# Performance work log

Measured on AMD Instinct MI355X. Metric: run time of the kernel, lower is better.

The kernel has to match this reference:

```python
import jax, jax.numpy as jnp
import numpy as np

N_NODES = 50000
N_EDGES = 800000
IN_DIM = 128
OUT_DIM = 64
LEAKY_SLOPE = 0.01  # torch F.leaky_relu default


def setup_inputs() -> dict:
    key = jax.random.key(0)
    k1, k2, k3, k4, k5 = jax.random.split(key, 5)
    features = jax.random.normal(k1, (N_NODES, IN_DIM), dtype=jnp.float32)
    src = jax.random.randint(k2, (N_EDGES,), 0, N_NODES, dtype=jnp.int32)
    dst = jax.random.randint(k3, (N_EDGES,), 0, N_NODES, dtype=jnp.int32)
    # fc: Linear(in_dim, out_dim, bias=False) -> stored as [in_dim, out_dim]
    W_fc = jax.random.normal(k4, (IN_DIM, OUT_DIM), dtype=jnp.float32) * (1.0 / np.sqrt(IN_DIM))
    # attn_fc: Linear(2*out_dim, 1, bias=False) -> stored as flat [2*out_dim]
    a_vec = jax.random.normal(k5, (2 * OUT_DIM,), dtype=jnp.float32) * (1.0 / np.sqrt(2 * OUT_DIM))
    return {"features": features, "src": src, "dst": dst, "W_fc": W_fc, "a_vec": a_vec}


def reference(features, src, dst, W_fc, a_vec):
    n = features.shape[0]
    d = W_fc.shape[1]
    # node projection: z = fc(features)
    z = features @ W_fc                                   # [N, d]
    # attn score: a^T [z_src || z_dst] = (z @ a_src)[src] + (z @ a_dst)[dst]
    az_src = z @ a_vec[:d]                                # [N]
    az_dst = z @ a_vec[d:]                                # [N]
    e = jax.nn.leaky_relu(az_src[src] + az_dst[dst], negative_slope=LEAKY_SLOPE)  # [E]
    # segment softmax over edges grouped by destination node
    e_max = jax.ops.segment_max(e, dst, num_segments=n)   # [N] (-inf for isolated nodes)
    e_exp = jnp.exp(e - e_max[dst])                       # [E]
    e_sum = jax.ops.segment_sum(e_exp, dst, num_segments=n)  # [N]
    alpha = e_exp / e_sum[dst]                            # [E]
    # weighted scatter-sum of source features to destination nodes
    h = jax.ops.segment_sum(alpha[:, None] * z[src], dst, num_segments=n)  # [N, d]
    return h
```

## Files before the change

kernel.cpp:

```cpp
#include <hip/hip_runtime.h>
#include <hip/hip_bf16.h>
#include <math.h>

#define N_NODES 50000
#define N_EDGES 800000
#define IN_DIM  128
#define OUT_DIM 64
#define LEAKY   0.01f

#define PROJ_ROWS 64
#define PROJ_NB   ((N_NODES + PROJ_ROWS - 1) / PROJ_ROWS)

#define SCAN_B   1024
#define SCAN_NB  ((N_NODES + SCAN_B - 1) / SCAN_B)

__global__ __launch_bounds__(256) void proj_kernel(
        const float* __restrict__ feat, const float* __restrict__ W,
        const float* __restrict__ a,
        __hip_bfloat16* __restrict__ zb,
        float* __restrict__ az_src, float* __restrict__ az_dst) {
    __shared__ float fs[PROJ_ROWS * IN_DIM];
    int tid  = threadIdx.x;
    int row0 = blockIdx.x * PROJ_ROWS;
    int nrows = N_NODES - row0; if (nrows > PROJ_ROWS) nrows = PROJ_ROWS;

    const float4* gsrc = (const float4*)(feat + (size_t)row0 * IN_DIM);
    if (nrows == PROJ_ROWS) {
#pragma unroll
        for (int i = 0; i < 8; ++i) {
            int idx = tid + i * 256;
            ((float4*)fs)[idx] = gsrc[idx];
        }
    } else {
        int lim = nrows * (IN_DIM / 4);
#pragma unroll
        for (int i = 0; i < 8; ++i) {
            int idx = tid + i * 256;
            if (idx < lim) ((float4*)fs)[idx] = gsrc[idx];
        }
    }
    __syncthreads();

    int lane  = tid & 63;
    int rbase = (tid >> 6) * 16;

    float acc[16];
#pragma unroll
    for (int r = 0; r < 16; ++r) acc[r] = 0.f;

    for (int kk = 0; kk < IN_DIM / 4; ++kk) {
        float w0 = W[(kk * 4 + 0) * OUT_DIM + lane];
        float w1 = W[(kk * 4 + 1) * OUT_DIM + lane];
        float w2 = W[(kk * 4 + 2) * OUT_DIM + lane];
        float w3 = W[(kk * 4 + 3) * OUT_DIM + lane];
#pragma unroll
        for (int r = 0; r < 16; ++r) {
            float4 f = *(const float4*)&fs[(rbase + r) * IN_DIM + kk * 4];
            acc[r] = fmaf(f.x, w0, acc[r]);
            acc[r] = fmaf(f.y, w1, acc[r]);
            acc[r] = fmaf(f.z, w2, acc[r]);
            acc[r] = fmaf(f.w, w3, acc[r]);
        }
    }

    float a1 = a[lane], a2 = a[OUT_DIM + lane];
#pragma unroll
    for (int r = 0; r < 16; ++r) {
        int row = row0 + rbase + r;
        if (row < N_NODES) {
            zb[(size_t)row * OUT_DIM + lane] = __float2bfloat16(acc[r]);
            float s1 = acc[r] * a1;
            float s2 = acc[r] * a2;
#pragma unroll
            for (int off = 32; off > 0; off >>= 1) {
                s1 += __shfl_xor(s1, off, 64);
                s2 += __shfl_xor(s2, off, 64);
            }
            if (lane == r) { az_src[row] = s1; az_dst[row] = s2; }
        }
    }
}

__global__ __launch_bounds__(256) void hist_kernel(
        const int* __restrict__ dst, int* __restrict__ counts,
        int* __restrict__ rank) {
    int i = blockIdx.x * 256 + threadIdx.x;
    if (i < N_EDGES) rank[i] = atomicAdd(&counts[dst[i]], 1);
}

__global__ __launch_bounds__(SCAN_B) void scan1_kernel(
        const int* __restrict__ counts, int* __restrict__ offsets,
        int* __restrict__ blocksums) {
    __shared__ int s[SCAN_B];
    int i = blockIdx.x * SCAN_B + threadIdx.x;
    int v = (i < N_NODES) ? counts[i] : 0;
    s[threadIdx.x] = v;
    __syncthreads();
    for (int off = 1; off < SCAN_B; off <<= 1) {
        int t = (threadIdx.x >= off) ? s[threadIdx.x - off] : 0;
        __syncthreads();
        s[threadIdx.x] += t;
        __syncthreads();
    }
    if (i < N_NODES) offsets[i] = s[threadIdx.x] - v;
    if (threadIdx.x == SCAN_B - 1) blocksums[blockIdx.x] = s[SCAN_B - 1];
}

__global__ __launch_bounds__(SCAN_B) void scan3_kernel(
        int* __restrict__ offsets, const int* __restrict__ blocksums) {
    __shared__ int bs[64];
    if (threadIdx.x < 64) {
        int lane = threadIdx.x;
        int v = (lane < SCAN_NB) ? blocksums[lane] : 0;
        int inc = v;
#pragma unroll
        for (int off = 1; off < 64; off <<= 1) {
            int t = __shfl_up(inc, off, 64);
            if (lane >= off) inc += t;
        }
        bs[lane] = inc - v;
    }
    __syncthreads();
    int i = blockIdx.x * SCAN_B + threadIdx.x;
    if (i < N_NODES) offsets[i] += bs[blockIdx.x];
    if (i == 0) offsets[N_NODES] = N_EDGES;
}

__global__ __launch_bounds__(256) void build_csr_kernel(
        const int* __restrict__ src, const int* __restrict__ dst,
        const int* __restrict__ rank, const int* __restrict__ offsets,
        int* __restrict__ src_sorted) {
    int i = blockIdx.x * 256 + threadIdx.x;
    if (i >= N_EDGES) return;
    int t = dst[i];
    int pos = offsets[t] + rank[i];
    src_sorted[pos] = src[i];
}

__global__ __launch_bounds__(256) void node_fused_kernel(
        const int* __restrict__ offsets, const int* __restrict__ src_sorted,
        const float* __restrict__ az_src, const float* __restrict__ az_dst,
        const __hip_bfloat16* __restrict__ zb, float* __restrict__ h) {
    int lane = threadIdx.x & 63;
    int w    = threadIdx.x >> 6;
    int t    = blockIdx.x * 4 + w;
    if (t >= N_NODES) return;
    int beg = offsets[t];
    int end = offsets[t + 1];
    float az_d = az_dst[t];

    float acc0 = 0.f, acc1 = 0.f, acc2 = 0.f, acc3 = 0.f;
    float ss0 = 0.f, ss1 = 0.f, ss2 = 0.f, ss3 = 0.f;
    int i = beg;
    for (; i + 4 <= end; i += 4) {
        int s0 = src_sorted[i];
        int s1 = src_sorted[i + 1];
        int s2 = src_sorted[i + 2];
        int s3 = src_sorted[i + 3];
        float v0 = az_src[s0] + az_d;
        float v1 = az_src[s1] + az_d;
        float v2 = az_src[s2] + az_d;
        float v3 = az_src[s3] + az_d;
        v0 = v0 > 0.f ? v0 : LEAKY * v0;
        v1 = v1 > 0.f ? v1 : LEAKY * v1;
        v2 = v2 > 0.f ? v2 : LEAKY * v2;
        v3 = v3 > 0.f ? v3 : LEAKY * v3;
        float x0 = __expf(v0), x1 = __expf(v1);
        float x2 = __expf(v2), x3 = __expf(v3);
        ss0 += x0; ss1 += x1; ss2 += x2; ss3 += x3;
        acc0 = fmaf(x0, __bfloat162float(zb[(size_t)s0 * OUT_DIM + lane]), acc0);
        acc1 = fmaf(x1, __bfloat162float(zb[(size_t)s1 * OUT_DIM + lane]), acc1);
        acc2 = fmaf(x2, __bfloat162float(zb[(size_t)s2 * OUT_DIM + lane]), acc2);
        acc3 = fmaf(x3, __bfloat162float(zb[(size_t)s3 * OUT_DIM + lane]), acc3);
    }
    for (; i < end; ++i) {
        int s0 = src_sorted[i];
        float v0 = az_src[s0] + az_d;
        v0 = v0 > 0.f ? v0 : LEAKY * v0;
        float x0 = __expf(v0);
        ss0 += x0;
        acc0 = fmaf(x0, __bfloat162float(zb[(size_t)s0 * OUT_DIM + lane]), acc0);
    }
    float ssum = (ss0 + ss1) + (ss2 + ss3);
    float inv  = (end > beg) ? 1.f / ssum : 0.f;
    h[(size_t)t * OUT_DIM + lane] = ((acc0 + acc1) + (acc2 + acc3)) * inv;
}

extern "C" void kernel_launch(void* const* d_in, const int* in_sizes, int n_in,
                              void* d_out, int out_size, void* d_ws, size_t ws_size,
                              hipStream_t stream) {
    const float* feat = (const float*)d_in[0];
    const int*   src  = (const int*)  d_in[1];
    const int*   dst  = (const int*)  d_in[2];
    const float* W    = (const float*)d_in[3];
    const float* a    = (const float*)d_in[4];
    float* h = (float*)d_out;

    float* az_src     = (float*)d_ws;
    float* az_dst     = az_src + N_NODES;
    int*   counts     = (int*)(az_dst + N_NODES);
    int*   offsets    = counts + N_NODES;
    int*   blocksums  = offsets + N_NODES + 1;
    int*   rank       = blocksums + 64;
    int*   src_sorted = rank + N_EDGES;
    __hip_bfloat16* zb = (__hip_bfloat16*)(src_sorted + N_EDGES);

    hipMemsetAsync(counts, 0, sizeof(int) * N_NODES, stream);

    int eblocks = (N_EDGES + 255) / 256;
    hist_kernel<<<eblocks, 256, 0, stream>>>(dst, counts, rank);
    scan1_kernel<<<SCAN_NB, SCAN_B, 0, stream>>>(counts, offsets, blocksums);
    scan3_kernel<<<SCAN_NB, SCAN_B, 0, stream>>>(offsets, blocksums);

    proj_kernel<<<PROJ_NB, 256, 0, stream>>>(feat, W, a, zb, az_src, az_dst);

    build_csr_kernel<<<eblocks, 256, 0, stream>>>(src, dst, rank, offsets,
                                                  src_sorted);

    node_fused_kernel<<<(N_NODES + 3) / 4, 256, 0, stream>>>(
        offsets, src_sorted, az_src, az_dst, zb, h);
}
```

Before: 202.1 us.

## Replace rank array with cursor atomics and batch neighbor index loads via shuffles

The CSR build no longer stores a per-edge rank from the histogram pass. It keeps a per-node cursor, initialized from the offsets, and atomically increments it in the build kernel, which removes the rank array write and read (about 3.2 MB each way). The node aggregation kernel now loads up to 64 neighbor indices and their az_src values with one coalesced load per lane and broadcasts them with shuffles, instead of every lane loading the same values. The cost is a second round of atomics and more shuffle instructions, and edge order inside each segment becomes nondeterministic, which changes floating-point summation order.

```diff
diff --git a/kernel.cpp b/kernel.cpp
--- a/kernel.cpp
+++ b/kernel.cpp
@@ -82,10 +82,9 @@
 }
 
 __global__ __launch_bounds__(256) void hist_kernel(
-        const int* __restrict__ dst, int* __restrict__ counts,
-        int* __restrict__ rank) {
+        const int* __restrict__ dst, int* __restrict__ counts) {
     int i = blockIdx.x * 256 + threadIdx.x;
-    if (i < N_EDGES) rank[i] = atomicAdd(&counts[dst[i]], 1);
+    if (i < N_EDGES) atomicAdd(&counts[dst[i]], 1);
 }
 
 __global__ __launch_bounds__(SCAN_B) void scan1_kernel(
@@ -107,7 +106,8 @@
 }
 
 __global__ __launch_bounds__(SCAN_B) void scan3_kernel(
-        int* __restrict__ offsets, const int* __restrict__ blocksums) {
+        int* __restrict__ offsets, int* __restrict__ cursor,
+        const int* __restrict__ blocksums) {
     __shared__ int bs[64];
     if (threadIdx.x < 64) {
         int lane = threadIdx.x;
@@ -122,18 +122,20 @@
     }
     __syncthreads();
     int i = blockIdx.x * SCAN_B + threadIdx.x;
-    if (i < N_NODES) offsets[i] += bs[blockIdx.x];
+    if (i < N_NODES) {
+        int o = offsets[i] + bs[blockIdx.x];
+        offsets[i] = o;
+        cursor[i]  = o;
+    }
     if (i == 0) offsets[N_NODES] = N_EDGES;
 }
 
 __global__ __launch_bounds__(256) void build_csr_kernel(
         const int* __restrict__ src, const int* __restrict__ dst,
-        const int* __restrict__ rank, const int* __restrict__ offsets,
-        int* __restrict__ src_sorted) {
+        int* __restrict__ cursor, int* __restrict__ src_sorted) {
     int i = blockIdx.x * 256 + threadIdx.x;
     if (i >= N_EDGES) return;
-    int t = dst[i];
-    int pos = offsets[t] + rank[i];
+    int pos = atomicAdd(&cursor[dst[i]], 1);
     src_sorted[pos] = src[i];
 }
 
@@ -145,41 +147,51 @@
     int w    = threadIdx.x >> 6;
     int t    = blockIdx.x * 4 + w;
     if (t >= N_NODES) return;
-    int beg = offsets[t];
-    int end = offsets[t + 1];
+    int beg = __builtin_amdgcn_readfirstlane(offsets[t]);
+    int end = __builtin_amdgcn_readfirstlane(offsets[t + 1]);
     float az_d = az_dst[t];
 
     float acc0 = 0.f, acc1 = 0.f, acc2 = 0.f, acc3 = 0.f;
     float ss0 = 0.f, ss1 = 0.f, ss2 = 0.f, ss3 = 0.f;
-    int i = beg;
-    for (; i + 4 <= end; i += 4) {
-        int s0 = src_sorted[i];
-        int s1 = src_sorted[i + 1];
-        int s2 = src_sorted[i + 2];
-        int s3 = src_sorted[i + 3];
-        float v0 = az_src[s0] + az_d;
-        float v1 = az_src[s1] + az_d;
-        float v2 = az_src[s2] + az_d;
-        float v3 = az_src[s3] + az_d;
-        v0 = v0 > 0.f ? v0 : LEAKY * v0;
-        v1 = v1 > 0.f ? v1 : LEAKY * v1;
-        v2 = v2 > 0.f ? v2 : LEAKY * v2;
-        v3 = v3 > 0.f ? v3 : LEAKY * v3;
-        float x0 = __expf(v0), x1 = __expf(v1);
-        float x2 = __expf(v2), x3 = __expf(v3);
-        ss0 += x0; ss1 += x1; ss2 += x2; ss3 += x3;
-        acc0 = fmaf(x0, __bfloat162float(zb[(size_t)s0 * OUT_DIM + lane]), acc0);
-        acc1 = fmaf(x1, __bfloat162float(zb[(size_t)s1 * OUT_DIM + lane]), acc1);
-        acc2 = fmaf(x2, __bfloat162float(zb[(size_t)s2 * OUT_DIM + lane]), acc2);
-        acc3 = fmaf(x3, __bfloat162float(zb[(size_t)s3 * OUT_DIM + lane]), acc3);
-    }
-    for (; i < end; ++i) {
-        int s0 = src_sorted[i];
-        float v0 = az_src[s0] + az_d;
-        v0 = v0 > 0.f ? v0 : LEAKY * v0;
-        float x0 = __expf(v0);
-        ss0 += x0;
-        acc0 = fmaf(x0, __bfloat162float(zb[(size_t)s0 * OUT_DIM + lane]), acc0);
+
+    for (int chunk = beg; chunk < end; chunk += 64) {
+        int m = end - chunk; if (m > 64) m = 64;
+        int   si = 0;
+        float av = 0.f;
+        if (lane < m) {
+            si = src_sorted[chunk + lane];
+            av = az_src[si];
+        }
+        int j = 0;
+        for (; j + 4 <= m; j += 4) {
+            int s0 = __shfl(si, j,     64);
+            int s1 = __shfl(si, j + 1, 64);
+            int s2 = __shfl(si, j + 2, 64);
+            int s3 = __shfl(si, j + 3, 64);
+            float v0 = __shfl(av, j,     64) + az_d;
+            float v1 = __shfl(av, j + 1, 64) + az_d;
+            float v2 = __shfl(av, j + 2, 64) + az_d;
+            float v3 = __shfl(av, j + 3, 64) + az_d;
+            v0 = v0 > 0.f ? v0 : LEAKY * v0;
+            v1 = v1 > 0.f ? v1 : LEAKY * v1;
+            v2 = v2 > 0.f ? v2 : LEAKY * v2;
+            v3 = v3 > 0.f ? v3 : LEAKY * v3;
+            float x0 = __expf(v0), x1 = __expf(v1);
+            float x2 = __expf(v2), x3 = __expf(v3);
+            ss0 += x0; ss1 += x1; ss2 += x2; ss3 += x3;
+            acc0 = fmaf(x0, __bfloat162float(zb[(size_t)s0 * OUT_DIM + lane]), acc0);
+            acc1 = fmaf(x1, __bfloat162float(zb[(size_t)s1 * OUT_DIM + lane]), acc1);
+            acc2 = fmaf(x2, __bfloat162float(zb[(size_t)s2 * OUT_DIM + lane]), acc2);
+            acc3 = fmaf(x3, __bfloat162float(zb[(size_t)s3 * OUT_DIM + lane]), acc3);
+        }
+        for (; j < m; ++j) {
+            int   s0 = __shfl(si, j, 64);
+            float v0 = __shfl(av, j, 64) + az_d;
+            v0 = v0 > 0.f ? v0 : LEAKY * v0;
+            float x0 = __expf(v0);
+            ss0 += x0;
+            acc0 = fmaf(x0, __bfloat162float(zb[(size_t)s0 * OUT_DIM + lane]), acc0);
+        }
     }
     float ssum = (ss0 + ss1) + (ss2 + ss3);
     float inv  = (end > beg) ? 1.f / ssum : 0.f;
@@ -200,22 +212,21 @@
     float* az_dst     = az_src + N_NODES;
     int*   counts     = (int*)(az_dst + N_NODES);
     int*   offsets    = counts + N_NODES;
-    int*   blocksums  = offsets + N_NODES + 1;
-    int*   rank       = blocksums + 64;
-    int*   src_sorted = rank + N_EDGES;
+    int*   cursor     = offsets + N_NODES + 1;
+    int*   blocksums  = cursor + N_NODES;
+    int*   src_sorted = blocksums + 64;
     __hip_bfloat16* zb = (__hip_bfloat16*)(src_sorted + N_EDGES);
 
     hipMemsetAsync(counts, 0, sizeof(int) * N_NODES, stream);
 
     int eblocks = (N_EDGES + 255) / 256;
-    hist_kernel<<<eblocks, 256, 0, stream>>>(dst, counts, rank);
+    hist_kernel<<<eblocks, 256, 0, stream>>>(dst, counts);
     scan1_kernel<<<SCAN_NB, SCAN_B, 0, stream>>>(counts, offsets, blocksums);
-    scan3_kernel<<<SCAN_NB, SCAN_B, 0, stream>>>(offsets, blocksums);
+    scan3_kernel<<<SCAN_NB, SCAN_B, 0, stream>>>(offsets, cursor, blocksums);
 
     proj_kernel<<<PROJ_NB, 256, 0, stream>>>(feat, W, a, zb, az_src, az_dst);
 
-    build_csr_kernel<<<eblocks, 256, 0, stream>>>(src, dst, rank, offsets,
-                                                  src_sorted);
+    build_csr_kernel<<<eblocks, 256, 0, stream>>>(src, dst, cursor, src_sorted);
 
     node_fused_kernel<<<(N_NODES + 3) / 4, 256, 0, stream>>>(
         offsets, src_sorted, az_src, az_dst, zb, h);
```

Result: slower. 230.0 us (+13.8%).
